# Kernel optimization log

Measured on AMD Instinct MI355X. Metric: run time of the kernel, lower is better.

Reference implementation:

```python
import jax, jax.numpy as jnp
import numpy as np

D_MODEL = 1024
H = 16
D_K = D_MODEL // H
NEG_INF = -1.0e9  # matches masked_fill value in the torch source


def setup_inputs() -> dict:
    key = jax.random.key(0)
    kq, kk, kv, kwq, kwk, kwv, kwo = jax.random.split(key, 7)
    B, S = 2, 2048
    query = jax.random.normal(kq, (B, S, D_MODEL), dtype=jnp.float32)
    key_t = jax.random.normal(kk, (B, S, D_MODEL), dtype=jnp.float32)
    value = jax.random.normal(kv, (B, S, D_MODEL), dtype=jnp.float32)
    # causal mask: 1 = attend, 0 = masked (masked_fill(mask == 0, -1e9))
    masked_val = jnp.tril(jnp.ones((S, S), dtype=jnp.int32))[None, None, :, :]
    scale = 1.0 / np.sqrt(D_MODEL)
    w_q = jax.random.normal(kwq, (D_MODEL, D_MODEL), dtype=jnp.float32) * scale
    w_k = jax.random.normal(kwk, (D_MODEL, D_MODEL), dtype=jnp.float32) * scale
    w_v = jax.random.normal(kwv, (D_MODEL, D_MODEL), dtype=jnp.float32) * scale
    w_o = jax.random.normal(kwo, (D_MODEL, D_MODEL), dtype=jnp.float32) * scale
    return {"query": query, "key": key_t, "value": value, "masked_val": masked_val,
            "w_q": w_q, "w_k": w_k, "w_v": w_v, "w_o": w_o}


def reference(query, key, value, masked_val, w_q, w_k, w_v, w_o):
    B, Sq, _ = query.shape
    Sk = key.shape[1]
    # nn.Linear(x) = x @ W.T; weights stored as [out, in]
    Q = (query @ w_q.T).reshape(B, Sq, H, D_K).transpose(0, 2, 1, 3)  # [B,H,Sq,Dk]
    K = (key @ w_k.T).reshape(B, Sk, H, D_K).transpose(0, 2, 1, 3)    # [B,H,Sk,Dk]
    V = (value @ w_v.T).reshape(B, Sk, H, D_K).transpose(0, 2, 1, 3)  # [B,H,Sk,Dk]
    scores = jnp.einsum("bhqd,bhkd->bhqk", Q, K) / jnp.sqrt(jnp.float32(D_K))
    scores = jnp.where(masked_val == 0, NEG_INF, scores)
    probs = jax.nn.softmax(scores, axis=-1)  # dropout p=0.0 -> identity
    ctx = jnp.einsum("bhqk,bhkd->bhqd", probs, V)  # [B,H,Sq,Dk]
    ctx = ctx.transpose(0, 2, 1, 3).reshape(B, Sq, H * D_K)
    return ctx @ w_o.T
```

## Files before the change

### kernel.cpp

```cpp
#include <hip/hip_runtime.h>
#include <hip/hip_bf16.h>
#include <type_traits>

using bf16x8_t = __attribute__((ext_vector_type(8))) __bf16;
using bf16x4_t = __attribute__((ext_vector_type(4))) __bf16;
using f32x4_t  = __attribute__((ext_vector_type(4))) float;

#define MFMA16(a, b, c) __builtin_amdgcn_mfma_f32_16x16x32_bf16((a), (b), (c), 0, 0, 0)

constexpr int BATCH   = 2;
constexpr int SEQ     = 2048;
constexpr int DMODEL  = 1024;
constexpr int DK      = 64;
constexpr int MTOT    = BATCH * SEQ;
constexpr float SCL2 = 0.125f * 1.44269504088896f;

typedef const __attribute__((address_space(1))) unsigned int ga_u32;
typedef __attribute__((address_space(3))) unsigned int ls_u32;
__device__ __forceinline__ void glds16(const void* g, void* l) {
    __builtin_amdgcn_global_load_lds((ga_u32*)g, (ls_u32*)l, 16, 0, 0);
}

__device__ __forceinline__ float exp2_fast(float x) {
    float r;
    asm volatile("v_exp_f32 %0, %1" : "=v"(r) : "v"(x));
    return r;
}

__device__ __forceinline__ bf16x8_t cvt8(const float* __restrict__ p) {
    f32x4_t a = *(const f32x4_t*)p;
    f32x4_t b = *(const f32x4_t*)(p + 4);
    bf16x8_t r;
    r[0] = (__bf16)a[0]; r[1] = (__bf16)a[1]; r[2] = (__bf16)a[2]; r[3] = (__bf16)a[3];
    r[4] = (__bf16)b[0]; r[5] = (__bf16)b[1]; r[6] = (__bf16)b[2]; r[7] = (__bf16)b[3];
    return r;
}

__global__ __launch_bounds__(256) void cvt_w_kernel(
    const float* __restrict__ w0, const float* __restrict__ w1,
    const float* __restrict__ w2, const float* __restrict__ w3, __bf16* __restrict__ dst)
{
    const float* srcs[4] = {w0, w1, w2, w3};
    const float* s = srcs[blockIdx.y];
    __bf16* d = dst + (size_t)blockIdx.y * (DMODEL * DMODEL);
    size_t i = ((size_t)blockIdx.x * 256 + threadIdx.x) * 8;
    *(bf16x8_t*)(d + i) = cvt8(s + i);
}

template<bool A_BF16, bool C_F32>
__device__ __forceinline__ void gemm_body(
    const void* __restrict__ Ap, const __bf16* __restrict__ Bt,
    void* __restrict__ Cp, int m0, int n0, float cscale)
{
    constexpr int K = DMODEL, N = DMODEL;
    constexpr int NSTEPS = K / 32;
    __shared__ __align__(16) char smem[2][16384];

    const int tid  = threadIdx.x;
    const int wave = tid >> 6, lane = tid & 63;
    const int wm = wave >> 1, wn = wave & 1;
    const int l15 = lane & 15, lhi = lane >> 4;

    auto glds_A_bf16 = [&](int k0, int buf) {
        const __bf16* Ab = (const __bf16*)Ap;
        #pragma unroll
        for (int i = 0; i < 2; ++i) {
            int cbase = i * 256 + wave * 64;
            int slot = cbase + lane;
            int row = slot >> 2, c = slot & 3;
            int cs = (c + 4 - ((row >> 1) & 3)) & 3;
            glds16(Ab + (size_t)(m0 + row) * K + k0 + cs * 8, smem[buf] + (size_t)cbase * 16);
        }
    };
    auto glds_B = [&](int k0, int buf) {
        #pragma unroll
        for (int i = 0; i < 2; ++i) {
            int cbase = i * 256 + wave * 64;
            int slot = cbase + lane;
            int row = slot >> 2, c = slot & 3;
            int cs = (c + 4 - ((row >> 1) & 3)) & 3;
            glds16(Bt + (size_t)(n0 + row) * K + k0 + cs * 8,
                   smem[buf] + 8192 + (size_t)cbase * 16);
        }
    };
    auto load_A_f32 = [&](int k0, f32x4_t (&ar)[4]) {
        const float* Af = (const float*)Ap;
        #pragma unroll
        for (int i = 0; i < 4; ++i) {
            int g = i * 256 + tid;
            int row = g >> 3, c = g & 7;
            ar[i] = *(const f32x4_t*)(Af + (size_t)(m0 + row) * K + k0 + c * 4);
        }
    };
    auto write_A_f32 = [&](const f32x4_t (&ar)[4], int buf) {
        __bf16* a_ls = (__bf16*)smem[buf];
        #pragma unroll
        for (int i = 0; i < 4; ++i) {
            int g = i * 256 + tid;
            int row = g >> 3, c = g & 7;
            int pc = ((c >> 1) + ((row >> 1) & 3)) & 3;
            bf16x4_t w;
            w[0] = (__bf16)ar[i][0]; w[1] = (__bf16)ar[i][1];
            w[2] = (__bf16)ar[i][2]; w[3] = (__bf16)ar[i][3];
            *(bf16x4_t*)(a_ls + row * 32 + pc * 8 + (c & 1) * 4) = w;
        }
    };

    f32x4_t acc[4][4] = {};

    {
        f32x4_t ar0[4];
        if constexpr (A_BF16) glds_A_bf16(0, 0);
        else                  load_A_f32(0, ar0);
        glds_B(0, 0);
        if constexpr (!A_BF16) write_A_f32(ar0, 0);
    }
    __syncthreads();

    for (int st = 0; st < NSTEPS; ++st) {
        const int cur = st & 1;
        const bool have_next = (st + 1 < NSTEPS);
        f32x4_t areg[4];
        if (have_next) {
            const int k1 = (st + 1) * 32;
            if constexpr (A_BF16) glds_A_bf16(k1, cur ^ 1);
            else                  load_A_f32(k1, areg);
            glds_B(k1, cur ^ 1);
        }

        const __bf16* a_ls = (const __bf16*)smem[cur];
        const __bf16* b_ls = (const __bf16*)(smem[cur] + 8192);
        bf16x8_t af[4], bfr[4];
        #pragma unroll
        for (int i = 0; i < 4; ++i) {
            int row = wm * 64 + i * 16 + l15;
            int lc = (lhi + (row >> 1)) & 3;
            af[i] = *(const bf16x8_t*)(a_ls + row * 32 + lc * 8);
        }
        #pragma unroll
        for (int j = 0; j < 4; ++j) {
            int row = wn * 64 + j * 16 + l15;
            int lc = (lhi + (row >> 1)) & 3;
            bfr[j] = *(const bf16x8_t*)(b_ls + row * 32 + lc * 8);
        }
        #pragma unroll
        for (int i = 0; i < 4; ++i)
            #pragma unroll
            for (int j = 0; j < 4; ++j)
                acc[i][j] = MFMA16(af[i], bfr[j], acc[i][j]);

        if (have_next) {
            if constexpr (!A_BF16) write_A_f32(areg, cur ^ 1);
            __syncthreads();
        }
    }

    #pragma unroll
    for (int i = 0; i < 4; ++i)
        #pragma unroll
        for (int j = 0; j < 4; ++j)
            #pragma unroll
            for (int r = 0; r < 4; ++r) {
                int row = m0 + wm * 64 + i * 16 + lhi * 4 + r;
                int col = n0 + wn * 64 + j * 16 + l15;
                float v = acc[i][j][r] * cscale;
                if constexpr (C_F32)
                    ((float*)Cp)[(size_t)row * N + col] = v;
                else
                    ((__bf16*)Cp)[(size_t)row * N + col] = (__bf16)v;
            }
}

__global__ __launch_bounds__(256) void proj_qkv_kernel(
    const float* __restrict__ xq, const float* __restrict__ xk, const float* __restrict__ xv,
    const __bf16* __restrict__ wc,
    __bf16* __restrict__ oq, __bf16* __restrict__ ok, __bf16* __restrict__ ov)
{
    int lid = blockIdx.x + 8 * blockIdx.y + 256 * blockIdx.z;
    int nid = (lid & 7) * 96 + (lid >> 3);
    int z = nid >> 8, rem = nid & 255;
    int m0 = (rem >> 3) * 128, n0 = (rem & 7) * 128;

    const float* A; const __bf16* Bt; __bf16* C; float cs;
    if (z == 0)      { A = xq; Bt = wc;                       C = oq; cs = SCL2; }
    else if (z == 1) { A = xk; Bt = wc + DMODEL * DMODEL;     C = ok; cs = 1.0f; }
    else             { A = xv; Bt = wc + 2 * DMODEL * DMODEL; C = ov; cs = 1.0f; }
    gemm_body<false, false>(A, Bt, C, m0, n0, cs);
}

__global__ __launch_bounds__(256) void proj_out_kernel(
    const __bf16* __restrict__ ctx, const __bf16* __restrict__ woc, float* __restrict__ out)
{
    int lid = blockIdx.x + 8 * blockIdx.y;
    int nid = (lid & 7) * 32 + (lid >> 3);
    gemm_body<true, true>(ctx, woc, out, (nid >> 3) * 128, (nid & 7) * 128, 1.0f);
}

__global__ __launch_bounds__(512, 2) void attn_kernel(
    const __bf16* __restrict__ Qm, const __bf16* __restrict__ Km,
    const __bf16* __restrict__ Vm, __bf16* __restrict__ Om)
{
    constexpr int LDV = 72, LDP = 72;
    __shared__ __bf16 k_sh[2][64 * 64];
    __shared__ __bf16 v_sh[2][64 * LDV];
    __shared__ __bf16 p_sh[8][16 * LDP];

    const int tid  = threadIdx.x;
    const int wave = tid >> 6, lane = tid & 63;
    const int l15 = lane & 15, lhi = lane >> 4;

    int old = blockIdx.x + 16 * blockIdx.y;
    int nid = (old & 7) * 64 + (old >> 3);
    const int bh = nid >> 4, x = nid & 15;
    const int p = ((bh >> 1) & 1) ? 15 - x : x;
    const int q0 = p * 128;
    const int b = bh >> 4, h = bh & 15;

    const __bf16* Qb = Qm + (size_t)b * SEQ * DMODEL + h * DK;
    const __bf16* Kb = Km + (size_t)b * SEQ * DMODEL + h * DK;
    const __bf16* Vb = Vm + (size_t)b * SEQ * DMODEL + h * DK;

    const int qbase = q0 + wave * 16;

    bf16x8_t qf[2];
    {
        const __bf16* qp = Qb + (size_t)(qbase + l15) * DMODEL + lhi * 8;
        qf[0] = *(const bf16x8_t*)qp;
        qf[1] = *(const bf16x8_t*)(qp + 32);
    }
    bf16x8_t onesf;
    #pragma unroll
    for (int j = 0; j < 8; ++j) onesf[j] = (__bf16)1.0f;

    f32x4_t acc[4] = {};
    f32x4_t acc_l = {};
    float m2[4] = {-INFINITY, -INFINITY, -INFINITY, -INFINITY};

    const int vrow = tid >> 3, vgrp = tid & 7;
    bf16x8_t vreg;

    auto stageK = [&](int kv0, int buf) {
        int row = tid >> 3, c = (tid & 7) ^ (row & 7);
        glds16(Kb + (size_t)(kv0 + row) * DMODEL + c * 8,
               (char*)k_sh[buf] + (size_t)tid * 16);
    };
    auto loadV = [&](int kv0) {
        vreg = *(const bf16x8_t*)(Vb + (size_t)(kv0 + vrow) * DMODEL + vgrp * 8);
    };
    auto writeV = [&](int buf) {
        int sh = (vrow + vgrp * 8) & 63;
        #pragma unroll
        for (int j = 0; j < 8; ++j) v_sh[buf][(vgrp * 8 + j) * LDV + sh] = vreg[j];
    };

    auto body = [&](auto needmask_c, int kv0, int cur) {
        constexpr bool NEEDMASK = decltype(needmask_c)::value;
        const __bf16* ks_buf = k_sh[cur];
        const __bf16* vs_buf = v_sh[cur];

        f32x4_t sf[4] = {};
        #pragma unroll
        for (int ks = 0; ks < 2; ++ks)
            #pragma unroll
            for (int n = 0; n < 4; ++n) {
                int row = n * 16 + l15;
                bf16x8_t kf = *(const bf16x8_t*)(ks_buf + row * 64 + (((ks * 4 + lhi) ^ (row & 7)) * 8));
                sf[n] = MFMA16(qf[ks], kf, sf[n]);
            }

        const int qrow_base = qbase + lhi * 4;
        float pmax[4];
        #pragma unroll
        for (int r = 0; r < 4; ++r) {
            float mx = -3.0e38f;
            #pragma unroll
            for (int n = 0; n < 4; ++n) {
                float sv = sf[n][r];
                if constexpr (NEEDMASK)
                    if (kv0 + n * 16 + l15 > qrow_base + r) sv = -1.0e30f;
                sf[n][r] = sv;
                mx = fmaxf(mx, sv);
            }
            pmax[r] = mx;
        }
        #pragma unroll
        for (int r = 0; r < 4; ++r)
            #pragma unroll
            for (int off = 1; off < 16; off <<= 1)
                pmax[r] = fmaxf(pmax[r], __shfl_xor(pmax[r], off, 64));

        bool grew = (pmax[0] > m2[0] + 8.f) || (pmax[1] > m2[1] + 8.f) ||
                    (pmax[2] > m2[2] + 8.f) || (pmax[3] > m2[3] + 8.f);
        if (__any((int)grew)) {
            #pragma unroll
            for (int r = 0; r < 4; ++r) {
                float mnew = fmaxf(m2[r], pmax[r]);
                float sfac = exp2_fast(m2[r] - mnew);
                m2[r] = mnew;
                acc_l[r] *= sfac;
                #pragma unroll
                for (int n = 0; n < 4; ++n) acc[n][r] *= sfac;
            }
        }

        #pragma unroll
        for (int r = 0; r < 4; ++r)
            #pragma unroll
            for (int n = 0; n < 4; ++n)
                sf[n][r] = exp2_fast(sf[n][r] - m2[r]);

        #pragma unroll
        for (int r = 0; r < 4; ++r)
            #pragma unroll
            for (int n = 0; n < 4; ++n)
                p_sh[wave][(lhi * 4 + r) * LDP + ((n * 16 + l15 + ((lhi >> 1) << 3)) & 63)]
                    = (__bf16)sf[n][r];

        #pragma unroll
        for (int ks = 0; ks < 2; ++ks) {
            bf16x8_t pa = *(const bf16x8_t*)(
                &p_sh[wave][l15 * LDP + ((ks * 32 + lhi * 8 + ((l15 >> 3) << 3)) & 63)]);
            acc_l = MFMA16(pa, onesf, acc_l);
            #pragma unroll
            for (int n = 0; n < 4; ++n) {
                int d = n * 16 + l15;
                int rot = (ks * 32 + lhi * 8 + ((d >> 3) << 3)) & 63;
                bf16x8_t vf = *(const bf16x8_t*)(vs_buf + d * LDV + rot);
                acc[n] = MFMA16(pa, vf, acc[n]);
            }
        }
    };

    stageK(0, 0);
    loadV(0);
    writeV(0);
    __syncthreads();

    for (int t = 0; t < 2 * p; ++t) {
        stageK((t + 1) * 64, (t & 1) ^ 1);
        loadV((t + 1) * 64);
        body(std::integral_constant<bool, false>{}, t * 64, t & 1);
        writeV((t & 1) ^ 1);
        __syncthreads();
    }
    {
        const int t = 2 * p;
        stageK((t + 1) * 64, (t & 1) ^ 1);
        loadV((t + 1) * 64);
        body(std::integral_constant<bool, true>{}, t * 64, t & 1);
        writeV((t & 1) ^ 1);
        __syncthreads();
        body(std::integral_constant<bool, true>{}, (t + 1) * 64, (t + 1) & 1);
    }

    __bf16* Ob = Om + (size_t)b * SEQ * DMODEL + h * DK;
    #pragma unroll
    for (int n = 0; n < 4; ++n)
        #pragma unroll
        for (int r = 0; r < 4; ++r) {
            int row = qbase + lhi * 4 + r;
            Ob[(size_t)row * DMODEL + n * 16 + l15] = (__bf16)(acc[n][r] / acc_l[r]);
        }
}

extern "C" void kernel_launch(void* const* d_in, const int* in_sizes, int n_in,
                              void* d_out, int out_size, void* d_ws, size_t ws_size,
                              hipStream_t stream)
{
    const float* q  = (const float*)d_in[0];
    const float* k  = (const float*)d_in[1];
    const float* v  = (const float*)d_in[2];
    const float* wq = (const float*)d_in[4];
    const float* wk = (const float*)d_in[5];
    const float* wv = (const float*)d_in[6];
    const float* wo = (const float*)d_in[7];
    float* out = (float*)d_out;

    const size_t mat = (size_t)MTOT * DMODEL;
    __bf16* Qw = (__bf16*)d_ws;
    __bf16* Kw = Qw + mat;
    __bf16* Vw = Kw + mat;
    __bf16* Cw = Vw + mat;
    __bf16* Wc = Cw + mat;

    dim3 blk(256);
    cvt_w_kernel<<<dim3(512, 4), blk, 0, stream>>>(wq, wk, wv, wo, Wc);
    proj_qkv_kernel<<<dim3(8, 32, 3), blk, 0, stream>>>(q, k, v, Wc, Qw, Kw, Vw);
    attn_kernel<<<dim3(16, 32), dim3(512), 0, stream>>>(Qw, Kw, Vw, Cw);
    proj_out_kernel<<<dim3(8, 32), blk, 0, stream>>>(Cw, Wc + 3 * DMODEL * DMODEL, out);
}
```

Before: 127.5 us.

## Pre-convert activations to bf16, triple-buffer GEMM pipeline, prioritize attention MFMA

Activations q/k/v are now converted to bf16 in a separate pass, folded into the weight-conversion kernel, so the QKV projection can stage A through direct global-to-LDS loads instead of loading fp32 into registers and converting. The GEMM body switches from double to triple buffering, with explicit vmcnt waits and raw barriers so two tiles are in flight while one is computed. The attention kernel raises wave priority around its MFMA blocks. In exchange there is an extra fp32 read and bf16 write of all three activations, more workspace, and 48KB of LDS per GEMM block, which may lower occupancy.

```diff
diff --git a/kernel.cpp b/kernel.cpp
--- a/kernel.cpp
+++ b/kernel.cpp
@@ -3,7 +3,6 @@
 #include <type_traits>
 
 using bf16x8_t = __attribute__((ext_vector_type(8))) __bf16;
-using bf16x4_t = __attribute__((ext_vector_type(4))) __bf16;
 using f32x4_t  = __attribute__((ext_vector_type(4))) float;
 
 #define MFMA16(a, b, c) __builtin_amdgcn_mfma_f32_16x16x32_bf16((a), (b), (c), 0, 0, 0)
@@ -36,43 +35,52 @@
     return r;
 }
 
-__global__ __launch_bounds__(256) void cvt_w_kernel(
+__global__ __launch_bounds__(256) void cvt_all_kernel(
+    const float* __restrict__ q, const float* __restrict__ k, const float* __restrict__ v,
     const float* __restrict__ w0, const float* __restrict__ w1,
-    const float* __restrict__ w2, const float* __restrict__ w3, __bf16* __restrict__ dst)
-{
-    const float* srcs[4] = {w0, w1, w2, w3};
-    const float* s = srcs[blockIdx.y];
-    __bf16* d = dst + (size_t)blockIdx.y * (DMODEL * DMODEL);
+    const float* __restrict__ w2, const float* __restrict__ w3,
+    __bf16* __restrict__ dstA, __bf16* __restrict__ dstW)
+{
+    const int y = blockIdx.y;
+    const float* src;
+    __bf16* dst;
+    if (y < 3) {
+        const float* a[3] = {q, k, v};
+        src = a[y];
+        dst = dstA + (size_t)y * (MTOT * DMODEL);
+    } else {
+        if (blockIdx.x >= 512) return;
+        const float* w[4] = {w0, w1, w2, w3};
+        src = w[y - 3];
+        dst = dstW + (size_t)(y - 3) * (DMODEL * DMODEL);
+    }
     size_t i = ((size_t)blockIdx.x * 256 + threadIdx.x) * 8;
-    *(bf16x8_t*)(d + i) = cvt8(s + i);
-}
-
-template<bool A_BF16, bool C_F32>
+    *(bf16x8_t*)(dst + i) = cvt8(src + i);
+}
+
+template<bool C_F32>
 __device__ __forceinline__ void gemm_body(
-    const void* __restrict__ Ap, const __bf16* __restrict__ Bt,
+    const __bf16* __restrict__ A, const __bf16* __restrict__ Bt,
     void* __restrict__ Cp, int m0, int n0, float cscale)
 {
     constexpr int K = DMODEL, N = DMODEL;
-    constexpr int NSTEPS = K / 32;
-    __shared__ __align__(16) char smem[2][16384];
+    constexpr int NS = K / 32;
+    __shared__ __align__(16) char smem[3][16384];
 
     const int tid  = threadIdx.x;
     const int wave = tid >> 6, lane = tid & 63;
     const int wm = wave >> 1, wn = wave & 1;
     const int l15 = lane & 15, lhi = lane >> 4;
 
-    auto glds_A_bf16 = [&](int k0, int buf) {
-        const __bf16* Ab = (const __bf16*)Ap;
+    auto stage = [&](int k0, int buf) {
         #pragma unroll
         for (int i = 0; i < 2; ++i) {
             int cbase = i * 256 + wave * 64;
             int slot = cbase + lane;
             int row = slot >> 2, c = slot & 3;
             int cs = (c + 4 - ((row >> 1) & 3)) & 3;
-            glds16(Ab + (size_t)(m0 + row) * K + k0 + cs * 8, smem[buf] + (size_t)cbase * 16);
-        }
-    };
-    auto glds_B = [&](int k0, int buf) {
+            glds16(A + (size_t)(m0 + row) * K + k0 + cs * 8, smem[buf] + (size_t)cbase * 16);
+        }
         #pragma unroll
         for (int i = 0; i < 2; ++i) {
             int cbase = i * 256 + wave * 64;
@@ -83,53 +91,12 @@
                    smem[buf] + 8192 + (size_t)cbase * 16);
         }
     };
-    auto load_A_f32 = [&](int k0, f32x4_t (&ar)[4]) {
-        const float* Af = (const float*)Ap;
-        #pragma unroll
-        for (int i = 0; i < 4; ++i) {
-            int g = i * 256 + tid;
-            int row = g >> 3, c = g & 7;
-            ar[i] = *(const f32x4_t*)(Af + (size_t)(m0 + row) * K + k0 + c * 4);
-        }
-    };
-    auto write_A_f32 = [&](const f32x4_t (&ar)[4], int buf) {
-        __bf16* a_ls = (__bf16*)smem[buf];
-        #pragma unroll
-        for (int i = 0; i < 4; ++i) {
-            int g = i * 256 + tid;
-            int row = g >> 3, c = g & 7;
-            int pc = ((c >> 1) + ((row >> 1) & 3)) & 3;
-            bf16x4_t w;
-            w[0] = (__bf16)ar[i][0]; w[1] = (__bf16)ar[i][1];
-            w[2] = (__bf16)ar[i][2]; w[3] = (__bf16)ar[i][3];
-            *(bf16x4_t*)(a_ls + row * 32 + pc * 8 + (c & 1) * 4) = w;
-        }
-    };
 
     f32x4_t acc[4][4] = {};
 
-    {
-        f32x4_t ar0[4];
-        if constexpr (A_BF16) glds_A_bf16(0, 0);
-        else                  load_A_f32(0, ar0);
-        glds_B(0, 0);
-        if constexpr (!A_BF16) write_A_f32(ar0, 0);
-    }
-    __syncthreads();
-
-    for (int st = 0; st < NSTEPS; ++st) {
-        const int cur = st & 1;
-        const bool have_next = (st + 1 < NSTEPS);
-        f32x4_t areg[4];
-        if (have_next) {
-            const int k1 = (st + 1) * 32;
-            if constexpr (A_BF16) glds_A_bf16(k1, cur ^ 1);
-            else                  load_A_f32(k1, areg);
-            glds_B(k1, cur ^ 1);
-        }
-
-        const __bf16* a_ls = (const __bf16*)smem[cur];
-        const __bf16* b_ls = (const __bf16*)(smem[cur] + 8192);
+    auto mfma_step = [&](int buf) {
+        const __bf16* a_ls = (const __bf16*)smem[buf];
+        const __bf16* b_ls = (const __bf16*)(smem[buf] + 8192);
         bf16x8_t af[4], bfr[4];
         #pragma unroll
         for (int i = 0; i < 4; ++i) {
@@ -148,12 +115,26 @@
             #pragma unroll
             for (int j = 0; j < 4; ++j)
                 acc[i][j] = MFMA16(af[i], bfr[j], acc[i][j]);
-
-        if (have_next) {
-            if constexpr (!A_BF16) write_A_f32(areg, cur ^ 1);
-            __syncthreads();
-        }
-    }
+    };
+
+    stage(0, 0);
+    stage(32, 1);
+
+    for (int t = 0; t < NS - 2; ++t) {
+        asm volatile("s_waitcnt vmcnt(4)" ::: "memory");
+        __builtin_amdgcn_s_barrier();
+        __builtin_amdgcn_sched_barrier(0);
+        stage((t + 2) * 32, (t + 2) % 3);
+        mfma_step(t % 3);
+    }
+    asm volatile("s_waitcnt vmcnt(4)" ::: "memory");
+    __builtin_amdgcn_s_barrier();
+    __builtin_amdgcn_sched_barrier(0);
+    mfma_step((NS - 2) % 3);
+    asm volatile("s_waitcnt vmcnt(0)" ::: "memory");
+    __builtin_amdgcn_s_barrier();
+    __builtin_amdgcn_sched_barrier(0);
+    mfma_step((NS - 1) % 3);
 
     #pragma unroll
     for (int i = 0; i < 4; ++i)
@@ -172,8 +153,7 @@
 }
 
 __global__ __launch_bounds__(256) void proj_qkv_kernel(
-    const float* __restrict__ xq, const float* __restrict__ xk, const float* __restrict__ xv,
-    const __bf16* __restrict__ wc,
+    const __bf16* __restrict__ act, const __bf16* __restrict__ wc,
     __bf16* __restrict__ oq, __bf16* __restrict__ ok, __bf16* __restrict__ ov)
 {
     int lid = blockIdx.x + 8 * blockIdx.y + 256 * blockIdx.z;
@@ -181,11 +161,13 @@
     int z = nid >> 8, rem = nid & 255;
     int m0 = (rem >> 3) * 128, n0 = (rem & 7) * 128;
 
-    const float* A; const __bf16* Bt; __bf16* C; float cs;
-    if (z == 0)      { A = xq; Bt = wc;                       C = oq; cs = SCL2; }
-    else if (z == 1) { A = xk; Bt = wc + DMODEL * DMODEL;     C = ok; cs = 1.0f; }
-    else             { A = xv; Bt = wc + 2 * DMODEL * DMODEL; C = ov; cs = 1.0f; }
-    gemm_body<false, false>(A, Bt, C, m0, n0, cs);
+    const __bf16* A = act + (size_t)z * (MTOT * DMODEL);
+    const __bf16* Bt = wc + (size_t)z * (DMODEL * DMODEL);
+    __bf16* C; float cs;
+    if (z == 0)      { C = oq; cs = SCL2; }
+    else if (z == 1) { C = ok; cs = 1.0f; }
+    else             { C = ov; cs = 1.0f; }
+    gemm_body<false>(A, Bt, C, m0, n0, cs);
 }
 
 __global__ __launch_bounds__(256) void proj_out_kernel(
@@ -193,7 +175,7 @@
 {
     int lid = blockIdx.x + 8 * blockIdx.y;
     int nid = (lid & 7) * 32 + (lid >> 3);
-    gemm_body<true, true>(ctx, woc, out, (nid >> 3) * 128, (nid & 7) * 128, 1.0f);
+    gemm_body<true>(ctx, woc, out, (nid >> 3) * 128, (nid & 7) * 128, 1.0f);
 }
 
 __global__ __launch_bounds__(512, 2) void attn_kernel(
@@ -259,6 +241,7 @@
         const __bf16* vs_buf = v_sh[cur];
 
         f32x4_t sf[4] = {};
+        __builtin_amdgcn_s_setprio(1);
         #pragma unroll
         for (int ks = 0; ks < 2; ++ks)
             #pragma unroll
@@ -267,6 +250,7 @@
                 bf16x8_t kf = *(const bf16x8_t*)(ks_buf + row * 64 + (((ks * 4 + lhi) ^ (row & 7)) * 8));
                 sf[n] = MFMA16(qf[ks], kf, sf[n]);
             }
+        __builtin_amdgcn_s_setprio(0);
 
         const int qrow_base = qbase + lhi * 4;
         float pmax[4];
@@ -316,6 +300,7 @@
                 p_sh[wave][(lhi * 4 + r) * LDP + ((n * 16 + l15 + ((lhi >> 1) << 3)) & 63)]
                     = (__bf16)sf[n][r];
 
+        __builtin_amdgcn_s_setprio(1);
         #pragma unroll
         for (int ks = 0; ks < 2; ++ks) {
             bf16x8_t pa = *(const bf16x8_t*)(
@@ -329,6 +314,7 @@
                 acc[n] = MFMA16(pa, vf, acc[n]);
             }
         }
+        __builtin_amdgcn_s_setprio(0);
     };
 
     stageK(0, 0);
@@ -382,10 +368,11 @@
     __bf16* Vw = Kw + mat;
     __bf16* Cw = Vw + mat;
     __bf16* Wc = Cw + mat;
+    __bf16* Aw = Wc + 4 * (size_t)(DMODEL * DMODEL);
 
     dim3 blk(256);
-    cvt_w_kernel<<<dim3(512, 4), blk, 0, stream>>>(wq, wk, wv, wo, Wc);
-    proj_qkv_kernel<<<dim3(8, 32, 3), blk, 0, stream>>>(q, k, v, Wc, Qw, Kw, Vw);
+    cvt_all_kernel<<<dim3(2048, 7), blk, 0, stream>>>(q, k, v, wq, wk, wv, wo, Aw, Wc);
+    proj_qkv_kernel<<<dim3(8, 32, 3), blk, 0, stream>>>(Aw, Wc, Qw, Kw, Vw);
     attn_kernel<<<dim3(16, 32), dim3(512), 0, stream>>>(Qw, Kw, Vw, Cw);
     proj_out_kernel<<<dim3(8, 32), blk, 0, stream>>>(Cw, Wc + 3 * DMODEL * DMODEL, out);
 }
```

Result: faster. 122.7 us (-3.7%).
